# Kernel optimization log

Measured on AMD Instinct MI355X. Metric: run time of the kernel, lower is better.

Reference implementation:

```python
import jax, jax.numpy as jnp
import numpy as np


def setup_inputs() -> dict:
    key = jax.random.key(0)
    ks = jax.random.split(key, 5)
    B, T, C = 2, 2048, 1024
    x = jax.random.normal(ks[0], (B, T, C), dtype=jnp.float32)
    Wqkv = jax.random.normal(ks[1], (C, 3 * C), dtype=jnp.float32) * (C ** -0.5)
    bqkv = jax.random.normal(ks[2], (3 * C,), dtype=jnp.float32) * 0.02
    Wproj = jax.random.normal(ks[3], (C, C), dtype=jnp.float32) * (C ** -0.5)
    bproj = jax.random.normal(ks[4], (C,), dtype=jnp.float32) * 0.02
    return {"x": x, "Wqkv": Wqkv, "bqkv": bqkv, "Wproj": Wproj, "bproj": bproj}


def reference(x, Wqkv, bqkv, Wproj, bproj):
    B, T, C = x.shape
    n_head = 16
    hd = C // n_head
    x_proj = x @ Wqkv + bqkv  # [B, T, 3C]
    # NOTE: source reshapes (B, T, C) -> (B, n_head, T, hd) directly (no transpose);
    # we replicate that exactly for faithfulness.
    q = x_proj[:, :, :C].reshape(B, n_head, T, hd)
    k = x_proj[:, :, C:2 * C].reshape(B, n_head, T, hd)
    v = x_proj[:, :, 2 * C:].reshape(B, n_head, T, hd)
    att = jnp.einsum('bhtd,bhsd->bhts', q, k) * (1.0 / jnp.sqrt(jnp.float32(hd)))
    causal = jnp.tril(jnp.ones((T, T), dtype=bool))  # True where allowed
    att = jnp.where(causal, att, jnp.float32(-jnp.inf))
    att = jax.nn.softmax(att, axis=-1)
    y = att @ v  # [B, H, T, hd]
    y = jnp.transpose(y, (0, 2, 1, 3)).reshape(B, T, C)
    return y @ Wproj + bproj
```

## Files before the change

### kernel.cpp

```cpp
#include <hip/hip_runtime.h>
#include <hip/hip_bf16.h>
#include <stdint.h>

typedef __hip_bfloat16 bf16;
typedef __attribute__((ext_vector_type(8))) short bf16x8;
typedef __attribute__((ext_vector_type(4))) float f32x4;

__device__ __forceinline__ bf16x8 ldsv8(const bf16* p) { return *(const bf16x8*)p; }

__device__ __forceinline__ short bf_bits(float f) {
  union { bf16 h; short s; } u; u.h = __float2bfloat16(f); return u.s;
}

#define ASYNC16(ldsdst, gsrc)                                                  \
  __builtin_amdgcn_global_load_lds(                                            \
      (const __attribute__((address_space(1))) void*)(gsrc),                   \
      (__attribute__((address_space(3))) void*)(ldsdst), 16, 0, 0)

__device__ __forceinline__ bool is_bf16(const void* p) {
  const uint32_t* w = (const uint32_t*)p;
  int cnt = 0;
#pragma unroll 8
  for (int i = 0; i < 64; ++i) {
    uint32_t e = (w[i] >> 7) & 0xffu;
    cnt += (e >= 100u && e <= 150u) ? 1 : 0;
  }
  return cnt >= 40;
}

__device__ __forceinline__ float load_f32(const void* p, size_t idx, bool b16) {
  return b16 ? __bfloat162float(((const bf16*)p)[idx]) : ((const float*)p)[idx];
}

__device__ __forceinline__ void cvtT_body(const void* in, bf16* out, int R,
                                          int Ccols, int bx, int by,
                                          bf16 (*tile)[33]) {
  const bool b16 = is_bf16(in);
  int tx = threadIdx.x & 31, ty = threadIdx.x >> 5;
  int c0 = bx * 32, r0 = by * 32;
#pragma unroll
  for (int i = 0; i < 32; i += 8)
    tile[ty + i][tx] = __float2bfloat16(load_f32(in, (size_t)(r0 + ty + i) * Ccols + c0 + tx, b16));
  __syncthreads();
#pragma unroll
  for (int i = 0; i < 32; i += 8)
    out[(size_t)(c0 + ty + i) * R + r0 + tx] = tile[tx][ty + i];
}

__global__ __launch_bounds__(256) void prep_k(const float* __restrict__ x,
                                              bf16* __restrict__ xb,
                                              const void* __restrict__ Wqkv,
                                              bf16* __restrict__ WqkvT,
                                              const void* __restrict__ Wproj,
                                              bf16* __restrict__ WprojT) {
  __shared__ __align__(16) bf16 tile[32][33];
  const int id = blockIdx.x;
  if (id < 2048) {
    size_t i = (size_t)id * 256 + threadIdx.x;
    const float4 f0 = ((const float4*)x)[i * 2];
    const float4 f1 = ((const float4*)x)[i * 2 + 1];
    bf16x8 pk = {bf_bits(f0.x), bf_bits(f0.y), bf_bits(f0.z), bf_bits(f0.w),
                 bf_bits(f1.x), bf_bits(f1.y), bf_bits(f1.z), bf_bits(f1.w)};
    ((bf16x8*)xb)[i] = pk;
  } else if (id < 5120) {
    int id2 = id - 2048;
    cvtT_body(Wqkv, WqkvT, 1024, 3072, id2 % 96, id2 / 96, tile);
  } else {
    int id3 = id - 5120;
    cvtT_body(Wproj, WprojT, 1024, 1024, id3 % 32, id3 / 32, tile);
  }
}

__global__ __launch_bounds__(256) void cvtT_k(const void* __restrict__ in,
                                              bf16* __restrict__ out,
                                              int R, int Ccols) {
  __shared__ __align__(16) bf16 tile[32][33];
  cvtT_body(in, out, R, Ccols, blockIdx.x, blockIdx.y, tile);
}

__global__ __launch_bounds__(256) void cvt_k(const float* __restrict__ in,
                                             bf16* __restrict__ out) {
  size_t i = (size_t)blockIdx.x * 256 + threadIdx.x;
  const float4 f0 = ((const float4*)in)[i * 2];
  const float4 f1 = ((const float4*)in)[i * 2 + 1];
  bf16x8 pk = {bf_bits(f0.x), bf_bits(f0.y), bf_bits(f0.z), bf_bits(f0.w),
               bf_bits(f1.x), bf_bits(f1.y), bf_bits(f1.z), bf_bits(f1.w)};
  ((bf16x8*)out)[i] = pk;
}

template <int MODE, int BN>
__global__ __launch_bounds__(256) void gemm128(
    const void* __restrict__ Araw, const bf16* __restrict__ BT,
    const void* __restrict__ biasraw, void* __restrict__ outv) {
  constexpr int K = 1024;
  constexpr int NBF = BN / 32;
  __shared__ __align__(16) bf16 As[128 * 32];
  __shared__ __align__(16) bf16 Bs[BN * 32];
  const int tid = threadIdx.x;
  const int wave = tid >> 6, lane = tid & 63;
  const int quad = lane >> 4, l16 = lane & 15;
  const int m0 = blockIdx.x * 128, n0 = blockIdx.y * BN;
  const int wm = (wave & 1) * 64, wn = (wave >> 1) * (BN / 2);
  const bool a16 = (MODE == 0) ? is_bf16(Araw) : true;
  const bool bias16 = is_bf16(biasraw);

  f32x4 acc[4][NBF] = {};

  for (int kt = 0; kt < K; kt += 32) {
    __syncthreads();
    if (MODE != 0 || a16) {
#pragma unroll
      for (int i = 0; i < 2; ++i) {
        int slot = i * 256 + tid;
        int row = slot >> 2, col = (slot & 3) << 3;
        ASYNC16(As + slot * 8, ((const bf16*)Araw) + (size_t)(m0 + row) * K + kt + col);
      }
#pragma unroll
      for (int i = 0; i < BN / 64; ++i) {
        int slot = i * 256 + tid;
        int row = slot >> 2, col = (slot & 3) << 3;
        ASYNC16(Bs + slot * 8, BT + (size_t)(n0 + row) * K + kt + col);
      }
    } else {
#pragma unroll
      for (int i = 0; i < 2; ++i) {
        int slot = i * 256 + tid;
        int row = slot >> 2, col = (slot & 3) << 3;
        const float* ap = ((const float*)Araw) + (size_t)(m0 + row) * K + kt + col;
        float4 f0 = *(const float4*)ap;
        float4 f1 = *(const float4*)(ap + 4);
        bf16x8 pk = {bf_bits(f0.x), bf_bits(f0.y), bf_bits(f0.z), bf_bits(f0.w),
                     bf_bits(f1.x), bf_bits(f1.y), bf_bits(f1.z), bf_bits(f1.w)};
        *(bf16x8*)(As + slot * 8) = pk;
        if (i * 256 < BN * 4)
          *(bf16x8*)(Bs + slot * 8) = *(const bf16x8*)(BT + (size_t)(n0 + row) * K + kt + col);
      }
    }
    __syncthreads();
    bf16x8 af[4], bfr[NBF];
#pragma unroll
    for (int i = 0; i < 4; ++i)
      af[i] = ldsv8(As + (wm + i * 16 + l16) * 32 + quad * 8);
#pragma unroll
    for (int j = 0; j < NBF; ++j)
      bfr[j] = ldsv8(Bs + (wn + j * 16 + l16) * 32 + quad * 8);
#pragma unroll
    for (int i = 0; i < 4; ++i)
#pragma unroll
      for (int j = 0; j < NBF; ++j)
        acc[i][j] = __builtin_amdgcn_mfma_f32_16x16x32_bf16(af[i], bfr[j], acc[i][j], 0, 0, 0);
  }

  float biasf[NBF];
#pragma unroll
  for (int j = 0; j < NBF; ++j)
    biasf[j] = load_f32(biasraw, n0 + wn + j * 16 + l16, bias16);

#pragma unroll
  for (int i = 0; i < 4; ++i)
#pragma unroll
    for (int j = 0; j < NBF; ++j) {
      int ng = n0 + wn + j * 16 + l16;
#pragma unroll
      for (int r = 0; r < 4; ++r) {
        int mg = m0 + wm + i * 16 + quad * 4 + r;
        float v = acc[i][j][r] + biasf[j];
        if (MODE == 1) {
          ((float*)outv)[(size_t)mg * 1024 + ng] = v;
        } else {
          ((bf16*)outv)[(size_t)mg * 3072 + ng] =
              __float2bfloat16(ng < 1024 ? v * 0.125f : v);
        }
      }
    }
}

__global__ __launch_bounds__(512) void attn_k(const bf16* __restrict__ xproj,
                                              bf16* __restrict__ Yb) {
  __shared__ __align__(16) bf16 Ks[128 * 72];
  __shared__ __align__(16) bf16 VTs[64 * 136];
  __shared__ __align__(16) bf16 Ps[8 * 16 * 136];

  const int tid = threadIdx.x;
  const int wave = tid >> 6, lane = tid & 63;
  const int quad = lane >> 4, l16 = lane & 15;
  const int pid = blockIdx.x;
  const int qtA = pid, qtB = 15 - pid;
  const int bh = blockIdx.y, b = bh >> 4, h = bh & 15;
  const size_t rowbase = (size_t)(b * 2048 + h * 128) * 3072;
  const int q0[2] = {qtA * 128, qtB * 128};

  bf16x8 aq[2][2];
#pragma unroll
  for (int t = 0; t < 2; ++t) {
    int sg = q0[t] + wave * 16 + l16;
    const bf16* qp = xproj + rowbase + (size_t)(sg >> 4) * 3072 + ((sg & 15) << 6);
#pragma unroll
    for (int ks = 0; ks < 2; ++ks)
      aq[t][ks] = *(const bf16x8*)(qp + ks * 32 + quad * 8);
  }

  f32x4 o[2][4] = {};
  float mrow[2][4], lrow[2][4];
#pragma unroll
  for (int t = 0; t < 2; ++t)
#pragma unroll
    for (int r = 0; r < 4; ++r) { mrow[t][r] = -1e30f; lrow[t][r] = 0.f; }

  bf16* Pw = Ps + wave * (16 * 136);

  const int slot0 = tid, slot1 = 512 + tid;
  const int sA = slot0 >> 3, blkA = slot0 & 7;
  const int sB = slot1 >> 3, blkB = slot1 & 7;

  bf16x8 kreg[2], vreg[2];
#define ISSUE_LOADS(stv)                                                        \
  {                                                                             \
    int sg0 = (stv)*128 + sA, sg1 = (stv)*128 + sB;                             \
    const bf16* b0 = xproj + rowbase + (size_t)(sg0 >> 4) * 3072 + ((sg0 & 15) << 6); \
    const bf16* b1 = xproj + rowbase + (size_t)(sg1 >> 4) * 3072 + ((sg1 & 15) << 6); \
    kreg[0] = *(const bf16x8*)(b0 + 1024 + blkA * 8);                           \
    vreg[0] = *(const bf16x8*)(b0 + 2048 + blkA * 8);                           \
    kreg[1] = *(const bf16x8*)(b1 + 1024 + blkB * 8);                           \
    vreg[1] = *(const bf16x8*)(b1 + 2048 + blkB * 8);                           \
  }

  ISSUE_LOADS(0);

  for (int st = 0; st <= qtB; ++st) {
    __syncthreads();
    {
      *(bf16x8*)(Ks + sA * 72 + blkA * 8) = kreg[0];
      const bf16* ve0 = (const bf16*)&vreg[0];
      const int ssw0 = sA ^ (blkA << 3);
#pragma unroll
      for (int j = 0; j < 8; ++j) VTs[(blkA * 8 + j) * 136 + ssw0] = ve0[j];
      *(bf16x8*)(Ks + sB * 72 + blkB * 8) = kreg[1];
      const bf16* ve1 = (const bf16*)&vreg[1];
      const int ssw1 = sB ^ (blkB << 3);
#pragma unroll
      for (int j = 0; j < 8; ++j) VTs[(blkB * 8 + j) * 136 + ssw1] = ve1[j];
    }
    if (st < qtB) ISSUE_LOADS(st + 1);
    __syncthreads();

    const bool doA = (st <= qtA);
#pragma unroll
    for (int t = 0; t < 2; ++t) {
      if (t == 0 && !doA) continue;
      const bool diag = (st == (t == 0 ? qtA : qtB));

      f32x4 sc[8] = {};
      __builtin_amdgcn_s_setprio(1);
#pragma unroll
      for (int ks = 0; ks < 2; ++ks)
#pragma unroll
        for (int j = 0; j < 8; ++j) {
          bf16x8 bk = ldsv8(Ks + (j * 16 + l16) * 72 + (ks * 4 + quad) * 8);
          sc[j] = __builtin_amdgcn_mfma_f32_16x16x32_bf16(aq[t][ks], bk, sc[j], 0, 0, 0);
        }
      __builtin_amdgcn_s_setprio(0);

#pragma unroll
      for (int r = 0; r < 4; ++r) {
        float vals[8];
        float mx = -1e30f;
        if (diag) {
          const int rloc = wave * 16 + quad * 4 + r;
#pragma unroll
          for (int j = 0; j < 8; ++j) {
            float v = sc[j][r];
            if ((j * 16 + l16) > rloc) v = -1e30f;
            vals[j] = v;
            mx = fmaxf(mx, v);
          }
        } else {
#pragma unroll
          for (int j = 0; j < 8; ++j) {
            float v = sc[j][r];
            vals[j] = v;
            mx = fmaxf(mx, v);
          }
        }
#pragma unroll
        for (int d = 1; d < 16; d <<= 1) mx = fmaxf(mx, __shfl_xor(mx, d, 64));
        const bool stable = __all(mx <= mrow[t][r]);
        float mnew, alpha = 1.0f;
        if (stable) {
          mnew = mrow[t][r];
        } else {
          mnew = fmaxf(mrow[t][r], mx);
          alpha = __expf(mrow[t][r] - mnew);
          mrow[t][r] = mnew;
        }
        float rs = 0.f;
#pragma unroll
        for (int j = 0; j < 8; ++j) {
          float p = __expf(vals[j] - mnew);
          vals[j] = p;
          rs += p;
        }
#pragma unroll
        for (int d = 1; d < 16; d <<= 1) rs += __shfl_xor(rs, d, 64);
        if (stable) {
          lrow[t][r] += rs;
        } else {
          lrow[t][r] = lrow[t][r] * alpha + rs;
#pragma unroll
          for (int j = 0; j < 4; ++j) o[t][j][r] *= alpha;
        }
        bf16* prow = Pw + (quad * 4 + r) * 136;
        const int psw = quad << 3;
#pragma unroll
        for (int j = 0; j < 8; ++j) prow[(j * 16 + l16) ^ psw] = __float2bfloat16(vals[j]);
      }

      __builtin_amdgcn_s_setprio(1);
#pragma unroll
      for (int ks = 0; ks < 4; ++ks) {
        bf16x8 ap = ldsv8(Pw + l16 * 136 + (((ks * 4 + quad) ^ (l16 >> 2)) << 3));
#pragma unroll
        for (int j = 0; j < 4; ++j) {
          int d = j * 16 + l16;
          bf16x8 bv = ldsv8(VTs + d * 136 + (((ks * 4 + quad) ^ (2 * j + (l16 >> 3))) << 3));
          o[t][j] = __builtin_amdgcn_mfma_f32_16x16x32_bf16(ap, bv, o[t][j], 0, 0, 0);
        }
      }
      __builtin_amdgcn_s_setprio(0);
    }
  }
#undef ISSUE_LOADS

  bf16* Yh = Yb + (size_t)b * 2097152 + h * 64;
#pragma unroll
  for (int t = 0; t < 2; ++t)
#pragma unroll
    for (int r = 0; r < 4; ++r) {
      int tt = q0[t] + wave * 16 + quad * 4 + r;
      float inv = 1.f / lrow[t][r];
#pragma unroll
      for (int j = 0; j < 4; ++j)
        Yh[(size_t)tt * 1024 + j * 16 + l16] = __float2bfloat16(o[t][j][r] * inv);
    }
}

extern "C" void kernel_launch(void* const* d_in, const int* in_sizes, int n_in,
                              void* d_out, int out_size, void* d_ws, size_t ws_size,
                              hipStream_t stream) {
  (void)out_size;
  const void* px     = d_in[0];
  const void* pWqkv  = (n_in > 1) ? d_in[1] : d_in[0];
  const void* pbqkv  = (n_in > 2) ? d_in[2] : d_in[0];
  const void* pWproj = (n_in > 3) ? d_in[3] : d_in[0];
  const void* pbproj = (n_in > 4) ? d_in[4] : d_in[0];
  for (int i = 0; i < n_in; ++i) {
    switch (in_sizes[i]) {
      case 4194304: px     = d_in[i]; break;
      case 3145728: pWqkv  = d_in[i]; break;
      case 3072:    pbqkv  = d_in[i]; break;
      case 1048576: pWproj = d_in[i]; break;
      case 1024:    pbproj = d_in[i]; break;
      default: break;
    }
  }

  char* ws = (char*)d_ws;
  bf16* xproj = (bf16*)(ws + 0);

  if (ws_size >= 41943040) {
    bf16* xb     = (bf16*)(ws + 25165824);
    bf16* WqkvT  = (bf16*)(ws + 33554432);
    bf16* WprojT = (bf16*)(ws + 39845888);
    bf16* Yb     = (bf16*)(ws + 27262976);

    prep_k<<<dim3(6144), 256, 0, stream>>>((const float*)px, xb, pWqkv, WqkvT,
                                           pWproj, WprojT);
    gemm128<0, 128><<<dim3(32, 24), 256, 0, stream>>>(xb, WqkvT, pbqkv, xproj);
    attn_k<<<dim3(8, 32), 512, 0, stream>>>(xproj, Yb);
    gemm128<1, 64><<<dim3(32, 16), 256, 0, stream>>>(Yb, WprojT, pbproj, d_out);
  } else if (ws_size >= 39845888) {
    bf16* xb     = (bf16*)(ws + 25165824);
    bf16* WqkvT  = (bf16*)(ws + 33554432);
    bf16* WprojT = (bf16*)(ws + 25165824);
    bf16* Yb     = (bf16*)(ws + 27262976);

    cvt_k<<<dim3(2048), 256, 0, stream>>>((const float*)px, xb);
    cvtT_k<<<dim3(96, 32), 256, 0, stream>>>(pWqkv, WqkvT, 1024, 3072);
    gemm128<0, 128><<<dim3(32, 24), 256, 0, stream>>>(xb, WqkvT, pbqkv, xproj);
    cvtT_k<<<dim3(32, 32), 256, 0, stream>>>(pWproj, WprojT, 1024, 1024);
    attn_k<<<dim3(8, 32), 512, 0, stream>>>(xproj, Yb);
    gemm128<1, 64><<<dim3(32, 16), 256, 0, stream>>>(Yb, WprojT, pbproj, d_out);
  } else {
    bf16* WqkvT  = (bf16*)(ws + 25165824);
    bf16* WprojT = (bf16*)(ws + 25165824);
    bf16* Yb     = (bf16*)(ws + 27262976);

    cvtT_k<<<dim3(96, 32), 256, 0, stream>>>(pWqkv, WqkvT, 1024, 3072);
    gemm128<0, 128><<<dim3(32, 24), 256, 0, stream>>>(px, WqkvT, pbqkv, xproj);
    cvtT_k<<<dim3(32, 32), 256, 0, stream>>>(pWproj, WprojT, 1024, 1024);
    attn_k<<<dim3(8, 32), 512, 0, stream>>>(xproj, Yb);
    gemm128<1, 64><<<dim3(32, 16), 256, 0, stream>>>(Yb, WprojT, pbproj, d_out);
  }
}
```

Measured before the change: 209.7 us.

## Swizzle workgroup order for L2 locality and simplify online softmax rescale

Remaps the linear block index in both the GEMM and attention kernels with a stride-8 swizzle, likely so that consecutively scheduled workgroups spread across XCDs share A/B tiles or heads in each chiplet's L2. The attention kernel also drops the wave-uniform 'stable max' branch and the separate diagonal-mask branch, always computing alpha and rescaling the accumulators. This trades a few extra exps and multiplies for less divergence and simpler control flow. The attention swizzle hardcodes a grid of 8 x 32.

```diff
diff --git a/kernel.cpp b/kernel.cpp
--- a/kernel.cpp
+++ b/kernel.cpp
@@ -99,7 +99,10 @@
   const int tid = threadIdx.x;
   const int wave = tid >> 6, lane = tid & 63;
   const int quad = lane >> 4, l16 = lane & 15;
-  const int m0 = blockIdx.x * 128, n0 = blockIdx.y * BN;
+  const int nwg = gridDim.x * gridDim.y;
+  const int lin = blockIdx.y * gridDim.x + blockIdx.x;
+  const int swz = (lin & 7) * (nwg >> 3) + (lin >> 3);
+  const int m0 = (swz % gridDim.x) * 128, n0 = (swz / gridDim.x) * BN;
   const int wm = (wave & 1) * 64, wn = (wave >> 1) * (BN / 2);
   const bool a16 = (MODE == 0) ? is_bf16(Araw) : true;
   const bool bias16 = is_bf16(biasraw);
@@ -184,9 +187,11 @@
   const int tid = threadIdx.x;
   const int wave = tid >> 6, lane = tid & 63;
   const int quad = lane >> 4, l16 = lane & 15;
-  const int pid = blockIdx.x;
+  const int lin = (int)blockIdx.y * 8 + (int)blockIdx.x;
+  const int swz = (lin & 7) * 32 + (lin >> 3);
+  const int pid = swz & 7;
   const int qtA = pid, qtB = 15 - pid;
-  const int bh = blockIdx.y, b = bh >> 4, h = bh & 15;
+  const int bh = swz >> 3, b = bh >> 4, h = bh & 15;
   const size_t rowbase = (size_t)(b * 2048 + h * 128) * 3072;
   const int q0[2] = {qtA * 128, qtB * 128};
 
@@ -263,36 +268,21 @@
 
 #pragma unroll
       for (int r = 0; r < 4; ++r) {
+        const int rloc = wave * 16 + quad * 4 + r;
         float vals[8];
         float mx = -1e30f;
-        if (diag) {
-          const int rloc = wave * 16 + quad * 4 + r;
-#pragma unroll
-          for (int j = 0; j < 8; ++j) {
-            float v = sc[j][r];
-            if ((j * 16 + l16) > rloc) v = -1e30f;
-            vals[j] = v;
-            mx = fmaxf(mx, v);
-          }
-        } else {
-#pragma unroll
-          for (int j = 0; j < 8; ++j) {
-            float v = sc[j][r];
-            vals[j] = v;
-            mx = fmaxf(mx, v);
-          }
+#pragma unroll
+        for (int j = 0; j < 8; ++j) {
+          float v = sc[j][r];
+          if (diag && (j * 16 + l16) > rloc) v = -1e30f;
+          vals[j] = v;
+          mx = fmaxf(mx, v);
         }
 #pragma unroll
         for (int d = 1; d < 16; d <<= 1) mx = fmaxf(mx, __shfl_xor(mx, d, 64));
-        const bool stable = __all(mx <= mrow[t][r]);
-        float mnew, alpha = 1.0f;
-        if (stable) {
-          mnew = mrow[t][r];
-        } else {
-          mnew = fmaxf(mrow[t][r], mx);
-          alpha = __expf(mrow[t][r] - mnew);
-          mrow[t][r] = mnew;
-        }
+        float mnew = fmaxf(mrow[t][r], mx);
+        float alpha = __expf(mrow[t][r] - mnew);
+        mrow[t][r] = mnew;
         float rs = 0.f;
 #pragma unroll
         for (int j = 0; j < 8; ++j) {
@@ -302,13 +292,9 @@
         }
 #pragma unroll
         for (int d = 1; d < 16; d <<= 1) rs += __shfl_xor(rs, d, 64);
-        if (stable) {
-          lrow[t][r] += rs;
-        } else {
-          lrow[t][r] = lrow[t][r] * alpha + rs;
-#pragma unroll
-          for (int j = 0; j < 4; ++j) o[t][j][r] *= alpha;
-        }
+        lrow[t][r] = lrow[t][r] * alpha + rs;
+#pragma unroll
+        for (int j = 0; j < 4; ++j) o[t][j][r] *= alpha;
         bf16* prow = Pw + (quad * 4 + r) * 136;
         const int psw = quad << 3;
 #pragma unroll
```

Result: no change. 207.1 us (-1.3%).
